# Optimization experiments

Measured on AMD Instinct MI355X. Metric: run time of the kernel, lower is better.

Reference implementation:

```python
import jax, jax.numpy as jnp
import numpy as np

CANVAS = 28      # canvas_size
P = 2            # num_paths
S = 3            # num_segments
PPP = S * 3 + 1  # points_per_path = 10
T = 32           # samples per bezier segment
SS = 2           # 2x2 = 4 supersamples per pixel (num_samples=4)
MARGIN = 2.0
TAU = 0.5        # anti-alias softness of coverage (differentiable rasterizer)
LATENT = 64
HIDDEN = 512


def _leaky(x):
    return jnp.where(x >= 0, x, 0.2 * x)


def _encoder(x, e_w1, e_b1, e_w2, e_b2, w_mu, b_mu, w_lv, b_lv):
    h = x.reshape(x.shape[0], -1)
    h = _leaky(h @ e_w1 + e_b1)
    h = _leaky(h @ e_w2 + e_b2)
    return h @ w_mu + b_mu, h @ w_lv + b_lv


def _decoder(z, d_w1, d_b1, d_w2, d_b2, p_w, p_b, wd_w, wd_b, a_w, a_b):
    B = z.shape[0]
    h = jax.nn.selu(z @ d_w1 + d_b1)
    h = jax.nn.selu(h @ d_w2 + d_b2)
    pts = jnp.tanh(h @ p_w + p_b).reshape(B, P, PPP, 2)
    pts = pts * (CANVAS / 2 - MARGIN) + CANVAS / 2
    # stack overlapping cubic segments: [B,P,S,4,2]
    cp = jnp.stack([pts[:, :, 3 * s:3 * s + 4, :] for s in range(S)], axis=2)
    widths = jax.nn.sigmoid(h @ wd_w + wd_b) * 2.0 + 1.0  # [B,P]
    alphas = jax.nn.sigmoid(h @ a_w + a_b)                # [B,P]
    return cp, widths, alphas


def _render(cp, widths, alphas):
    """Differentiable supersampled stroke rasterizer, white bg, 1-x flip."""
    B = cp.shape[0]
    t = (jnp.arange(T, dtype=cp.dtype) + 0.5) / T
    basis = jnp.stack([(1 - t) ** 3, 3 * t * (1 - t) ** 2,
                       3 * t ** 2 * (1 - t), t ** 3], axis=-1)  # [T,4]
    curve = jnp.einsum('tk,bpskc->bpstc', basis, cp).reshape(B, P, S * T, 2)
    # supersampled pixel sample positions (pixel units)
    coords = (jnp.arange(CANVAS * SS, dtype=cp.dtype) + 0.5) / SS
    ys, xs = jnp.meshgrid(coords, coords, indexing='ij')
    samp = jnp.stack([xs, ys], -1).reshape(-1, 2)  # [N,2], N = (28*2)^2
    # [B,P,N,M] squared distances -> min over curve samples
    d2 = jnp.sum((samp[None, None, :, None, :] - curve[:, :, None, :, :]) ** 2, -1)
    d = jnp.sqrt(jnp.min(d2, axis=-1) + 1e-12)  # [B,P,N]
    cov = jax.nn.sigmoid((widths[..., None] * 0.5 - d) / TAU)
    a = alphas[..., None] * cov                 # per-path ink opacity
    val = jnp.prod(1.0 - a, axis=1)             # composite black ink over bg=1.0
    img = val.reshape(B, CANVAS, SS, CANVAS, SS).mean(axis=(2, 4))
    return 1.0 - img[:, None]                   # [B,1,H,W]


def setup_inputs() -> dict:
    key = jax.random.key(0)
    ks = jax.random.split(key, 24)
    n = lambda k, s, sc=0.05: (jax.random.normal(k, s, dtype=jnp.float32) * sc)
    B = 128
    return {
        'x': jax.random.uniform(ks[0], (B, 1, 28, 28), dtype=jnp.float32),
        'eps': jax.random.normal(ks[1], (B, LATENT), dtype=jnp.float32),
        'e_w1': n(ks[2], (784, 256)), 'e_b1': jnp.zeros(256),
        'e_w2': n(ks[3], (256, 256)), 'e_b2': jnp.zeros(256),
        'w_mu': n(ks[4], (256, LATENT)), 'b_mu': jnp.zeros(LATENT),
        'w_lv': n(ks[5], (256, LATENT)), 'b_lv': jnp.zeros(LATENT),
        'd_w1': n(ks[6], (LATENT, HIDDEN)), 'd_b1': jnp.zeros(HIDDEN),
        'd_w2': n(ks[7], (HIDDEN, HIDDEN)), 'd_b2': jnp.zeros(HIDDEN),
        'p_w': n(ks[8], (HIDDEN, P * PPP * 2)), 'p_b': jnp.zeros(P * PPP * 2),
        'wd_w': n(ks[9], (HIDDEN, P)), 'wd_b': jnp.zeros(P),
        'a_w': n(ks[10], (HIDDEN, P)), 'a_b': jnp.zeros(P),
    }


def reference(x, eps, e_w1, e_b1, e_w2, e_b2, w_mu, b_mu, w_lv, b_lv,
              d_w1, d_b1, d_w2, d_b2, p_w, p_b, wd_w, wd_b, a_w, a_b):
    mu, logvar = _encoder(x, e_w1, e_b1, e_w2, e_b2, w_mu, b_mu, w_lv, b_lv)
    z = mu + eps * jnp.exp(0.5 * logvar)
    cp, widths, alphas = _decoder(z, d_w1, d_b1, d_w2, d_b2,
                                  p_w, p_b, wd_w, wd_b, a_w, a_b)
    rendered = _render(cp, widths, alphas)
    return rendered, mu, logvar, cp, widths, alphas
```

## Files before the change

kernel.cpp:

```cpp
#include <hip/hip_runtime.h>
#include <hip/hip_bf16.h>
#include <math.h>

#define REND_OFF 0
#define MU_OFF   100352
#define LV_OFF   108544
#define CP_OFF   116736
#define W_OFF    122880
#define A_OFF    123136

#define Q_W1 0
#define Q_W2 25600
#define Q_ML 33792
#define Q_D1 37888
#define Q_D2 41984
#define Q_H  74752
#define Q_TOT 78848

__device__ __forceinline__ float leakyf(float x) {
    return x >= 0.f ? x : 0.2f * x;
}
__device__ __forceinline__ float seluf(float x) {
    const float sc = 1.0507009873554805f;
    const float al = 1.6732632423543772f;
    return x > 0.f ? sc * x : sc * al * expm1f(x);
}
__device__ __forceinline__ float sigmoidf(float x) {
    return 1.f / (1.f + expf(-x));
}
__device__ __forceinline__ void bf2(unsigned u, float& lo, float& hi) {
    lo = __uint_as_float(u << 16);
    hi = __uint_as_float(u & 0xffff0000u);
}
__device__ __forceinline__ unsigned short bfbits(float v) {
    __hip_bfloat16 h = (__hip_bfloat16)v;
    return *(unsigned short*)&h;
}

__global__ __launch_bounds__(256) void conv_w(
    const float* __restrict__ e_w1, const float* __restrict__ e_w2,
    const float* __restrict__ w_mu, const float* __restrict__ w_lv,
    const float* __restrict__ d_w1, const float* __restrict__ d_w2,
    const float* __restrict__ p_w,  const float* __restrict__ wd_w,
    const float* __restrict__ a_w,  uint4* __restrict__ wsq)
{
    int t = blockIdx.x * 256 + threadIdx.x;
    if (t >= Q_TOT) return;
    float v[8];
    if (t < Q_W2) {
        int q = t, k2 = q >> 6, j4 = q & 63;
        int k0 = 2 * k2, c0 = 4 * j4;
        #pragma unroll
        for (int e = 0; e < 8; ++e) {
            int k = k0 + (e >> 2), c = c0 + (e & 3);
            v[e] = (k < 784) ? e_w1[k * 256 + c] : 0.f;
        }
    } else if (t < Q_ML) {
        int q = t - Q_W2, k2 = q >> 6, j4 = q & 63;
        int k0 = 2 * k2, c0 = 4 * j4;
        #pragma unroll
        for (int e = 0; e < 8; ++e)
            v[e] = e_w2[(k0 + (e >> 2)) * 256 + c0 + (e & 3)];
    } else if (t < Q_D1) {
        int q = t - Q_ML, k2 = q >> 5, j4 = q & 31;
        int k0 = 2 * k2, c0 = 4 * j4;
        #pragma unroll
        for (int e = 0; e < 8; ++e) {
            int k = k0 + (e >> 2), c = c0 + (e & 3);
            v[e] = (c < 64) ? w_mu[k * 64 + c] : w_lv[k * 64 + c - 64];
        }
    } else if (t < Q_D2) {
        int q = t - Q_D1, k2 = q >> 7, j4 = q & 127;
        int k0 = 2 * k2, c0 = 4 * j4;
        #pragma unroll
        for (int e = 0; e < 8; ++e)
            v[e] = d_w1[(k0 + (e >> 2)) * 512 + c0 + (e & 3)];
    } else if (t < Q_H) {
        int q = t - Q_D2, k2 = q >> 7, j4 = q & 127;
        int k0 = 2 * k2, c0 = 4 * j4;
        #pragma unroll
        for (int e = 0; e < 8; ++e)
            v[e] = d_w2[(k0 + (e >> 2)) * 512 + c0 + (e & 3)];
    } else {
        int q = t - Q_H, k2 = q >> 4, j4 = q & 15;
        int k0 = 2 * k2, c0 = 4 * j4;
        #pragma unroll
        for (int e = 0; e < 8; ++e) {
            int k = k0 + (e >> 2), c = c0 + (e & 3);
            v[e] = (c < 40) ? p_w[k * 40 + c]
                 : (c < 42) ? wd_w[k * 2 + c - 40]
                 : (c < 44) ? a_w[k * 2 + c - 42] : 0.f;
        }
    }
    uint4 u;
    u.x = bfbits(v[0]) | ((unsigned)bfbits(v[1]) << 16);
    u.y = bfbits(v[2]) | ((unsigned)bfbits(v[3]) << 16);
    u.z = bfbits(v[4]) | ((unsigned)bfbits(v[5]) << 16);
    u.w = bfbits(v[6]) | ((unsigned)bfbits(v[7]) << 16);
    wsq[t] = u;
}

template<int K2, int N, int JG, int S, int KsP>
__device__ __forceinline__ void layer_gemm(const uint4* __restrict__ wq,
                                           const float4* __restrict__ xq,
                                           float* __restrict__ red, int tid)
{
    constexpr int NTp = N + 4;
    const int jg = tid % JG, ks = tid / JG;
    const uint4* wp = wq + (ks * KsP) * (N / 4) + jg;
    const float4* xp = xq + ks * KsP;
    float a00=0,a01=0,a02=0,a03=0, a10=0,a11=0,a12=0,a13=0;
    #pragma unroll 8
    for (int kk = 0; kk < KsP; ++kk) {
        uint4 w = wp[kk * (N / 4)];
        float4 xv = xp[kk];
        float w0,w1,w2,w3,w4,w5,w6,w7;
        bf2(w.x,w0,w1); bf2(w.y,w2,w3); bf2(w.z,w4,w5); bf2(w.w,w6,w7);
        a00=fmaf(xv.x,w0,a00); a01=fmaf(xv.x,w1,a01);
        a02=fmaf(xv.x,w2,a02); a03=fmaf(xv.x,w3,a03);
        a10=fmaf(xv.y,w0,a10); a11=fmaf(xv.y,w1,a11);
        a12=fmaf(xv.y,w2,a12); a13=fmaf(xv.y,w3,a13);
        a00=fmaf(xv.z,w4,a00); a01=fmaf(xv.z,w5,a01);
        a02=fmaf(xv.z,w6,a02); a03=fmaf(xv.z,w7,a03);
        a10=fmaf(xv.w,w4,a10); a11=fmaf(xv.w,w5,a11);
        a12=fmaf(xv.w,w6,a12); a13=fmaf(xv.w,w7,a13);
    }
    *(float4*)&red[(0 * S + ks) * NTp + 4 * jg] = make_float4(a00,a01,a02,a03);
    *(float4*)&red[(1 * S + ks) * NTp + 4 * jg] = make_float4(a10,a11,a12,a13);
}

template<int N, int S, int ACT>
__device__ __forceinline__ void layer_reduce(const float* __restrict__ red,
                                             const float* __restrict__ bias,
                                             float* __restrict__ Cint, int tid)
{
    constexpr int NTp = N + 4;
    if (tid < 2 * N) {
        int b = tid / N, j = tid % N;
        float s = bias[j];
        #pragma unroll
        for (int si = 0; si < S; ++si) s += red[(b * S + si) * NTp + j];
        s = (ACT == 1) ? leakyf(s) : seluf(s);
        Cint[j * 2 + b] = s;
    }
}

__global__ __launch_bounds__(1024) void vae_mlp(
    const float* __restrict__ x,    const float* __restrict__ eps,
    const float* __restrict__ e_b1, const float* __restrict__ e_b2,
    const float* __restrict__ b_mu, const float* __restrict__ b_lv,
    const float* __restrict__ d_b1, const float* __restrict__ d_b2,
    const float* __restrict__ p_b,  const float* __restrict__ wd_b,
    const float* __restrict__ a_b,
    const uint4* __restrict__ wsq,  float* __restrict__ out)
{
    const int b0  = blockIdx.x * 2;
    const int tid = threadIdx.x;

    __shared__ __align__(16) float xs[1600];
    __shared__ __align__(16) float h1i[512];
    __shared__ __align__(16) float h2i[512];
    __shared__ __align__(16) float zsi[128];
    __shared__ __align__(16) float hd1i[1024];
    __shared__ __align__(16) float hd2i[1024];
    __shared__ float mulv[2][128];
    __shared__ float pts[2][40];
    __shared__ __align__(16) float red[8704];

    for (int i = tid; i < 1600; i += 1024) {
        int k = i >> 1, b = i & 1;
        xs[i] = (k < 784) ? x[(b0 + b) * 784 + k] : 0.f;
    }
    __syncthreads();

    layer_gemm<400, 256, 64, 16, 25>(wsq + Q_W1, (const float4*)xs, red, tid);
    __syncthreads();
    layer_reduce<256, 16, 1>(red, e_b1, h1i, tid);
    __syncthreads();

    layer_gemm<128, 256, 64, 16, 8>(wsq + Q_W2, (const float4*)h1i, red, tid);
    __syncthreads();
    layer_reduce<256, 16, 1>(red, e_b2, h2i, tid);
    __syncthreads();

    layer_gemm<128, 128, 32, 32, 4>(wsq + Q_ML, (const float4*)h2i, red, tid);
    __syncthreads();
    if (tid < 256) {
        int b = tid >> 7, u = tid & 127;
        float s = (u < 64) ? b_mu[u] : b_lv[u - 64];
        #pragma unroll
        for (int si = 0; si < 32; ++si) s += red[(b * 32 + si) * 132 + u];
        mulv[b][u] = s;
        out[(u < 64 ? MU_OFF : LV_OFF) + (b0 + b) * 64 + (u & 63)] = s;
    }
    __syncthreads();
    if (tid < 128) {
        int b = tid >> 6, j = tid & 63;
        zsi[j * 2 + b] = fmaf(eps[(b0 + b) * 64 + j],
                              expf(0.5f * mulv[b][64 + j]), mulv[b][j]);
    }
    __syncthreads();

    layer_gemm<32, 512, 128, 8, 4>(wsq + Q_D1, (const float4*)zsi, red, tid);
    __syncthreads();
    layer_reduce<512, 8, 2>(red, d_b1, hd1i, tid);
    __syncthreads();

    layer_gemm<256, 512, 128, 8, 32>(wsq + Q_D2, (const float4*)hd1i, red, tid);
    __syncthreads();
    layer_reduce<512, 8, 2>(red, d_b2, hd2i, tid);
    __syncthreads();

    layer_gemm<256, 64, 16, 64, 4>(wsq + Q_H, (const float4*)hd2i, red, tid);
    __syncthreads();
    if (tid < 128) {
        int b = tid >> 6, u = tid & 63;
        if (u < 44) {
            float s = 0.f;
            #pragma unroll
            for (int si = 0; si < 64; ++si) s += red[(b * 64 + si) * 68 + u];
            if (u < 40) {
                pts[b][u] = tanhf(s + p_b[u]) * 12.f + 14.f;
            } else if (u < 42) {
                out[W_OFF + (b0 + b) * 2 + (u - 40)] =
                    sigmoidf(s + wd_b[u - 40]) * 2.f + 1.f;
            } else {
                out[A_OFF + (b0 + b) * 2 + (u - 42)] = sigmoidf(s + a_b[u - 42]);
            }
        }
    }
    __syncthreads();

    if (tid < 96) {
        int bs = tid / 48, i = tid % 48;
        int p = i / 24, rem = i % 24;
        int s = rem / 8, kc = rem % 8;
        int k = kc >> 1, c = kc & 1;
        out[CP_OFF + (b0 + bs) * 48 + i] = pts[bs][p * 20 + (3 * s + k) * 2 + c];
    }
}

__global__ __launch_bounds__(256) void vae_render(float* __restrict__ out)
{
    const int b   = blockIdx.x;
    const int q   = blockIdx.y;
    const int tid = threadIdx.x;

    __shared__ float2 cur[192];
    __shared__ float  wa[4];

    if (tid < 192) {
        int p = tid / 96;
        int m = tid % 96;
        int s = m / 32;
        int t = m % 32;
        float u  = (t + 0.5f) * (1.f / 32.f);
        float v  = 1.f - u;
        float b0 = v * v * v;
        float b1 = 3.f * u * v * v;
        float b2 = 3.f * u * u * v;
        float b3 = u * u * u;
        const float* cp = out + CP_OFF + b * 48 + p * 24 + s * 8;
        float cx = b0 * cp[0] + b1 * cp[2] + b2 * cp[4] + b3 * cp[6];
        float cy = b0 * cp[1] + b1 * cp[3] + b2 * cp[5] + b3 * cp[7];
        cur[tid] = make_float2(cx, cy);
    } else if (tid < 196) {
        int i = tid - 192;
        wa[i] = (i < 2) ? 0.5f * out[W_OFF + b * 2 + i]
                        : out[A_OFF + b * 2 + (i - 2)];
    }
    __syncthreads();

    if (tid < 196) {
        int Y = tid / 28, X = tid - Y * 28;
        float px0 = X + 0.25f;
        float py0 = (7 * q + Y) + 0.25f;

        float mA[4] = {1e30f, 1e30f, 1e30f, 1e30f};
        float mB[4] = {1e30f, 1e30f, 1e30f, 1e30f};
        #pragma unroll 4
        for (int m = 0; m < 96; ++m) {
            float2 c = cur[m];
            float dx0 = px0 - c.x, dy0 = py0 - c.y;
            float dx1 = dx0 + 0.5f, dy1 = dy0 + 0.5f;
            float xx0 = dx0 * dx0, xx1 = dx1 * dx1;
            float yy0 = dy0 * dy0, yy1 = dy1 * dy1;
            mA[0] = fminf(mA[0], xx0 + yy0);
            mA[1] = fminf(mA[1], xx1 + yy0);
            mA[2] = fminf(mA[2], xx0 + yy1);
            mA[3] = fminf(mA[3], xx1 + yy1);
        }
        #pragma unroll 4
        for (int m = 96; m < 192; ++m) {
            float2 c = cur[m];
            float dx0 = px0 - c.x, dy0 = py0 - c.y;
            float dx1 = dx0 + 0.5f, dy1 = dy0 + 0.5f;
            float xx0 = dx0 * dx0, xx1 = dx1 * dx1;
            float yy0 = dy0 * dy0, yy1 = dy1 * dy1;
            mB[0] = fminf(mB[0], xx0 + yy0);
            mB[1] = fminf(mB[1], xx1 + yy0);
            mB[2] = fminf(mB[2], xx0 + yy1);
            mB[3] = fminf(mB[3], xx1 + yy1);
        }

        const float w0 = wa[0], w1 = wa[1], a0 = wa[2], a1 = wa[3];
        float v = 0.f;
        #pragma unroll
        for (int s = 0; s < 4; ++s) {
            float d0 = sqrtf(mA[s] + 1e-12f);
            float d1 = sqrtf(mB[s] + 1e-12f);
            float c0 = a0 / (1.f + expf(-2.f * (w0 - d0)));
            float c1 = a1 / (1.f + expf(-2.f * (w1 - d1)));
            v += (1.f - c0) * (1.f - c1);
        }
        out[REND_OFF + b * 784 + (7 * q + Y) * 28 + X] = 1.f - 0.25f * v;
    }
}

extern "C" void kernel_launch(void* const* d_in, const int* in_sizes, int n_in,
                              void* d_out, int out_size, void* d_ws, size_t ws_size,
                              hipStream_t stream) {
    const float* x    = (const float*)d_in[0];
    const float* eps  = (const float*)d_in[1];
    const float* e_w1 = (const float*)d_in[2];
    const float* e_b1 = (const float*)d_in[3];
    const float* e_w2 = (const float*)d_in[4];
    const float* e_b2 = (const float*)d_in[5];
    const float* w_mu = (const float*)d_in[6];
    const float* b_mu = (const float*)d_in[7];
    const float* w_lv = (const float*)d_in[8];
    const float* b_lv = (const float*)d_in[9];
    const float* d_w1 = (const float*)d_in[10];
    const float* d_b1 = (const float*)d_in[11];
    const float* d_w2 = (const float*)d_in[12];
    const float* d_b2 = (const float*)d_in[13];
    const float* p_w  = (const float*)d_in[14];
    const float* p_b  = (const float*)d_in[15];
    const float* wd_w = (const float*)d_in[16];
    const float* wd_b = (const float*)d_in[17];
    const float* a_w  = (const float*)d_in[18];
    const float* a_b  = (const float*)d_in[19];
    float* out = (float*)d_out;
    uint4* wsq = (uint4*)d_ws;

    hipLaunchKernelGGL(conv_w, dim3((Q_TOT + 255) / 256), dim3(256), 0, stream,
                       e_w1, e_w2, w_mu, w_lv, d_w1, d_w2, p_w, wd_w, a_w, wsq);
    hipLaunchKernelGGL(vae_mlp, dim3(64), dim3(1024), 0, stream,
                       x, eps, e_b1, e_b2, b_mu, b_lv, d_b1, d_b2,
                       p_b, wd_b, a_b, wsq, out);
    hipLaunchKernelGGL(vae_render, dim3(128, 4), dim3(256), 0, stream, out);
}
```

Baseline: 125.5 us.

## Switch MLP to fp16 packed dot2 and process one sample per block

Weights are now stored as fp16 pairs along K instead of bf16 pairs along N. Activations are packed into fp16 pairs, and the GEMM inner loop uses the v_dot2 fp32-accumulate intrinsic. Each block now handles one batch sample instead of two, which doubles the grid to 128 blocks and halves per-block work and shared memory. This is meant to cut ALU work and spread the serial MLP chain across more CUs, but weight traffic per sample doubles and fp16 range and precision differ from bf16.

```diff
diff --git a/kernel.cpp b/kernel.cpp
--- a/kernel.cpp
+++ b/kernel.cpp
@@ -1,5 +1,6 @@
 #include <hip/hip_runtime.h>
 #include <hip/hip_bf16.h>
+#include <hip/hip_fp16.h>
 #include <math.h>
 
 #define REND_OFF 0
@@ -17,6 +18,8 @@
 #define Q_H  74752
 #define Q_TOT 78848
 
+typedef _Float16 half2_t __attribute__((ext_vector_type(2)));
+
 __device__ __forceinline__ float leakyf(float x) {
     return x >= 0.f ? x : 0.2f * x;
 }
@@ -28,13 +31,21 @@
 __device__ __forceinline__ float sigmoidf(float x) {
     return 1.f / (1.f + expf(-x));
 }
-__device__ __forceinline__ void bf2(unsigned u, float& lo, float& hi) {
-    lo = __uint_as_float(u << 16);
-    hi = __uint_as_float(u & 0xffff0000u);
-}
-__device__ __forceinline__ unsigned short bfbits(float v) {
-    __hip_bfloat16 h = (__hip_bfloat16)v;
-    return *(unsigned short*)&h;
+__device__ __forceinline__ unsigned pkh(float a, float b) {
+    __half ha = __float2half(a), hb = __float2half(b);
+    return (unsigned)__half_as_ushort(ha) | ((unsigned)__half_as_ushort(hb) << 16);
+}
+__device__ __forceinline__ half2_t as_h2(unsigned u) {
+    union { unsigned u; half2_t h; } c; c.u = u; return c.h;
+}
+__device__ __forceinline__ float dot2(unsigned a, unsigned w, float acc) {
+#if __has_builtin(__builtin_amdgcn_fdot2)
+    return __builtin_amdgcn_fdot2(as_h2(a), as_h2(w), acc, false);
+#else
+    half2_t ah = as_h2(a), wh = as_h2(w);
+    acc = fmaf((float)ah[0], (float)wh[0], acc);
+    return fmaf((float)ah[1], (float)wh[1], acc);
+#endif
 }
 
 __global__ __launch_bounds__(256) void conv_w(
@@ -46,102 +57,110 @@
 {
     int t = blockIdx.x * 256 + threadIdx.x;
     if (t >= Q_TOT) return;
-    float v[8];
+    float lo[4], hi[4];
     if (t < Q_W2) {
         int q = t, k2 = q >> 6, j4 = q & 63;
         int k0 = 2 * k2, c0 = 4 * j4;
         #pragma unroll
-        for (int e = 0; e < 8; ++e) {
-            int k = k0 + (e >> 2), c = c0 + (e & 3);
-            v[e] = (k < 784) ? e_w1[k * 256 + c] : 0.f;
+        for (int c = 0; c < 4; ++c) {
+            lo[c] = (k0     < 784) ? e_w1[k0 * 256 + c0 + c] : 0.f;
+            hi[c] = (k0 + 1 < 784) ? e_w1[(k0 + 1) * 256 + c0 + c] : 0.f;
         }
     } else if (t < Q_ML) {
         int q = t - Q_W2, k2 = q >> 6, j4 = q & 63;
         int k0 = 2 * k2, c0 = 4 * j4;
         #pragma unroll
-        for (int e = 0; e < 8; ++e)
-            v[e] = e_w2[(k0 + (e >> 2)) * 256 + c0 + (e & 3)];
+        for (int c = 0; c < 4; ++c) {
+            lo[c] = e_w2[k0 * 256 + c0 + c];
+            hi[c] = e_w2[(k0 + 1) * 256 + c0 + c];
+        }
     } else if (t < Q_D1) {
         int q = t - Q_ML, k2 = q >> 5, j4 = q & 31;
         int k0 = 2 * k2, c0 = 4 * j4;
         #pragma unroll
-        for (int e = 0; e < 8; ++e) {
-            int k = k0 + (e >> 2), c = c0 + (e & 3);
-            v[e] = (c < 64) ? w_mu[k * 64 + c] : w_lv[k * 64 + c - 64];
+        for (int c = 0; c < 4; ++c) {
+            int cc = c0 + c;
+            lo[c] = (cc < 64) ? w_mu[k0 * 64 + cc] : w_lv[k0 * 64 + cc - 64];
+            hi[c] = (cc < 64) ? w_mu[(k0 + 1) * 64 + cc]
+                              : w_lv[(k0 + 1) * 64 + cc - 64];
         }
     } else if (t < Q_D2) {
         int q = t - Q_D1, k2 = q >> 7, j4 = q & 127;
         int k0 = 2 * k2, c0 = 4 * j4;
         #pragma unroll
-        for (int e = 0; e < 8; ++e)
-            v[e] = d_w1[(k0 + (e >> 2)) * 512 + c0 + (e & 3)];
+        for (int c = 0; c < 4; ++c) {
+            lo[c] = d_w1[k0 * 512 + c0 + c];
+            hi[c] = d_w1[(k0 + 1) * 512 + c0 + c];
+        }
     } else if (t < Q_H) {
         int q = t - Q_D2, k2 = q >> 7, j4 = q & 127;
         int k0 = 2 * k2, c0 = 4 * j4;
         #pragma unroll
-        for (int e = 0; e < 8; ++e)
-            v[e] = d_w2[(k0 + (e >> 2)) * 512 + c0 + (e & 3)];
+        for (int c = 0; c < 4; ++c) {
+            lo[c] = d_w2[k0 * 512 + c0 + c];
+            hi[c] = d_w2[(k0 + 1) * 512 + c0 + c];
+        }
     } else {
         int q = t - Q_H, k2 = q >> 4, j4 = q & 15;
         int k0 = 2 * k2, c0 = 4 * j4;
         #pragma unroll
-        for (int e = 0; e < 8; ++e) {
-            int k = k0 + (e >> 2), c = c0 + (e & 3);
-            v[e] = (c < 40) ? p_w[k * 40 + c]
-                 : (c < 42) ? wd_w[k * 2 + c - 40]
-                 : (c < 44) ? a_w[k * 2 + c - 42] : 0.f;
+        for (int c = 0; c < 4; ++c) {
+            int cc = c0 + c;
+            lo[c] = (cc < 40) ? p_w[k0 * 40 + cc]
+                  : (cc < 42) ? wd_w[k0 * 2 + cc - 40]
+                  : (cc < 44) ? a_w[k0 * 2 + cc - 42] : 0.f;
+            hi[c] = (cc < 40) ? p_w[(k0 + 1) * 40 + cc]
+                  : (cc < 42) ? wd_w[(k0 + 1) * 2 + cc - 40]
+                  : (cc < 44) ? a_w[(k0 + 1) * 2 + cc - 42] : 0.f;
         }
     }
     uint4 u;
-    u.x = bfbits(v[0]) | ((unsigned)bfbits(v[1]) << 16);
-    u.y = bfbits(v[2]) | ((unsigned)bfbits(v[3]) << 16);
-    u.z = bfbits(v[4]) | ((unsigned)bfbits(v[5]) << 16);
-    u.w = bfbits(v[6]) | ((unsigned)bfbits(v[7]) << 16);
+    u.x = pkh(lo[0], hi[0]);
+    u.y = pkh(lo[1], hi[1]);
+    u.z = pkh(lo[2], hi[2]);
+    u.w = pkh(lo[3], hi[3]);
     wsq[t] = u;
 }
 
-template<int K2, int N, int JG, int S, int KsP>
-__device__ __forceinline__ void layer_gemm(const uint4* __restrict__ wq,
-                                           const float4* __restrict__ xq,
-                                           float* __restrict__ red, int tid)
+template<int N, int JG, int S, int Ks>
+__device__ __forceinline__ void hgemm(const uint4* __restrict__ wq,
+                                      const unsigned* __restrict__ xu,
+                                      float* __restrict__ red, int tid)
 {
     constexpr int NTp = N + 4;
     const int jg = tid % JG, ks = tid / JG;
-    const uint4* wp = wq + (ks * KsP) * (N / 4) + jg;
-    const float4* xp = xq + ks * KsP;
-    float a00=0,a01=0,a02=0,a03=0, a10=0,a11=0,a12=0,a13=0;
+    const uint4* wp = wq + (ks * Ks) * (N / 4) + jg;
+    const unsigned* xp = xu + ks * Ks;
+    float a0 = 0.f, a1 = 0.f, a2 = 0.f, a3 = 0.f;
     #pragma unroll 8
-    for (int kk = 0; kk < KsP; ++kk) {
+    for (int kk = 0; kk < Ks; ++kk) {
         uint4 w = wp[kk * (N / 4)];
-        float4 xv = xp[kk];
-        float w0,w1,w2,w3,w4,w5,w6,w7;
-        bf2(w.x,w0,w1); bf2(w.y,w2,w3); bf2(w.z,w4,w5); bf2(w.w,w6,w7);
-        a00=fmaf(xv.x,w0,a00); a01=fmaf(xv.x,w1,a01);
-        a02=fmaf(xv.x,w2,a02); a03=fmaf(xv.x,w3,a03);
-        a10=fmaf(xv.y,w0,a10); a11=fmaf(xv.y,w1,a11);
-        a12=fmaf(xv.y,w2,a12); a13=fmaf(xv.y,w3,a13);
-        a00=fmaf(xv.z,w4,a00); a01=fmaf(xv.z,w5,a01);
-        a02=fmaf(xv.z,w6,a02); a03=fmaf(xv.z,w7,a03);
-        a10=fmaf(xv.w,w4,a10); a11=fmaf(xv.w,w5,a11);
-        a12=fmaf(xv.w,w6,a12); a13=fmaf(xv.w,w7,a13);
-    }
-    *(float4*)&red[(0 * S + ks) * NTp + 4 * jg] = make_float4(a00,a01,a02,a03);
-    *(float4*)&red[(1 * S + ks) * NTp + 4 * jg] = make_float4(a10,a11,a12,a13);
+        unsigned av = xp[kk];
+        a0 = dot2(av, w.x, a0);
+        a1 = dot2(av, w.y, a1);
+        a2 = dot2(av, w.z, a2);
+        a3 = dot2(av, w.w, a3);
+    }
+    *(float4*)&red[ks * NTp + 4 * jg] = make_float4(a0, a1, a2, a3);
 }
 
 template<int N, int S, int ACT>
-__device__ __forceinline__ void layer_reduce(const float* __restrict__ red,
-                                             const float* __restrict__ bias,
-                                             float* __restrict__ Cint, int tid)
+__device__ __forceinline__ void reduce_pack(const float* __restrict__ red,
+                                            const float* __restrict__ bias,
+                                            unsigned* __restrict__ Cu, int tid)
 {
     constexpr int NTp = N + 4;
-    if (tid < 2 * N) {
-        int b = tid / N, j = tid % N;
-        float s = bias[j];
-        #pragma unroll
-        for (int si = 0; si < S; ++si) s += red[(b * S + si) * NTp + j];
-        s = (ACT == 1) ? leakyf(s) : seluf(s);
-        Cint[j * 2 + b] = s;
+    if (tid < N / 2) {
+        int j0 = 2 * tid;
+        float s0 = bias[j0], s1 = bias[j0 + 1];
+        #pragma unroll
+        for (int si = 0; si < S; ++si) {
+            s0 += red[si * NTp + j0];
+            s1 += red[si * NTp + j0 + 1];
+        }
+        if (ACT == 1) { s0 = leakyf(s0); s1 = leakyf(s1); }
+        else          { s0 = seluf(s0);  s1 = seluf(s1);  }
+        Cu[tid] = pkh(s0, s1);
     }
 }
 
@@ -154,89 +173,94 @@
     const float* __restrict__ a_b,
     const uint4* __restrict__ wsq,  float* __restrict__ out)
 {
-    const int b0  = blockIdx.x * 2;
+    const int b   = blockIdx.x;
     const int tid = threadIdx.x;
 
-    __shared__ __align__(16) float xs[1600];
-    __shared__ __align__(16) float h1i[512];
-    __shared__ __align__(16) float h2i[512];
-    __shared__ __align__(16) float zsi[128];
-    __shared__ __align__(16) float hd1i[1024];
-    __shared__ __align__(16) float hd2i[1024];
-    __shared__ float mulv[2][128];
-    __shared__ float pts[2][40];
-    __shared__ __align__(16) float red[8704];
-
-    for (int i = tid; i < 1600; i += 1024) {
-        int k = i >> 1, b = i & 1;
-        xs[i] = (k < 784) ? x[(b0 + b) * 784 + k] : 0.f;
-    }
-    __syncthreads();
-
-    layer_gemm<400, 256, 64, 16, 25>(wsq + Q_W1, (const float4*)xs, red, tid);
-    __syncthreads();
-    layer_reduce<256, 16, 1>(red, e_b1, h1i, tid);
-    __syncthreads();
-
-    layer_gemm<128, 256, 64, 16, 8>(wsq + Q_W2, (const float4*)h1i, red, tid);
-    __syncthreads();
-    layer_reduce<256, 16, 1>(red, e_b2, h2i, tid);
-    __syncthreads();
-
-    layer_gemm<128, 128, 32, 32, 4>(wsq + Q_ML, (const float4*)h2i, red, tid);
-    __syncthreads();
-    if (tid < 256) {
-        int b = tid >> 7, u = tid & 127;
-        float s = (u < 64) ? b_mu[u] : b_lv[u - 64];
-        #pragma unroll
-        for (int si = 0; si < 32; ++si) s += red[(b * 32 + si) * 132 + u];
-        mulv[b][u] = s;
-        out[(u < 64 ? MU_OFF : LV_OFF) + (b0 + b) * 64 + (u & 63)] = s;
-    }
-    __syncthreads();
-    if (tid < 128) {
-        int b = tid >> 6, j = tid & 63;
-        zsi[j * 2 + b] = fmaf(eps[(b0 + b) * 64 + j],
-                              expf(0.5f * mulv[b][64 + j]), mulv[b][j]);
-    }
-    __syncthreads();
-
-    layer_gemm<32, 512, 128, 8, 4>(wsq + Q_D1, (const float4*)zsi, red, tid);
-    __syncthreads();
-    layer_reduce<512, 8, 2>(red, d_b1, hd1i, tid);
-    __syncthreads();
-
-    layer_gemm<256, 512, 128, 8, 32>(wsq + Q_D2, (const float4*)hd1i, red, tid);
-    __syncthreads();
-    layer_reduce<512, 8, 2>(red, d_b2, hd2i, tid);
-    __syncthreads();
-
-    layer_gemm<256, 64, 16, 64, 4>(wsq + Q_H, (const float4*)hd2i, red, tid);
-    __syncthreads();
-    if (tid < 128) {
-        int b = tid >> 6, u = tid & 63;
-        if (u < 44) {
-            float s = 0.f;
-            #pragma unroll
-            for (int si = 0; si < 64; ++si) s += red[(b * 64 + si) * 68 + u];
-            if (u < 40) {
-                pts[b][u] = tanhf(s + p_b[u]) * 12.f + 14.f;
-            } else if (u < 42) {
-                out[W_OFF + (b0 + b) * 2 + (u - 40)] =
-                    sigmoidf(s + wd_b[u - 40]) * 2.f + 1.f;
-            } else {
-                out[A_OFF + (b0 + b) * 2 + (u - 42)] = sigmoidf(s + a_b[u - 42]);
-            }
-        }
-    }
-    __syncthreads();
-
-    if (tid < 96) {
-        int bs = tid / 48, i = tid % 48;
-        int p = i / 24, rem = i % 24;
+    __shared__ __align__(16) unsigned xs[400];
+    __shared__ __align__(16) unsigned h1u[128];
+    __shared__ __align__(16) unsigned h2u[128];
+    __shared__ __align__(16) unsigned zu[32];
+    __shared__ __align__(16) unsigned d1u[256];
+    __shared__ __align__(16) unsigned d2u[256];
+    __shared__ float mulv[128];
+    __shared__ float pts[40];
+    __shared__ __align__(16) float red[4352];
+
+    if (tid < 400) {
+        int k0 = 2 * tid;
+        float x0 = (k0     < 784) ? x[b * 784 + k0] : 0.f;
+        float x1 = (k0 + 1 < 784) ? x[b * 784 + k0 + 1] : 0.f;
+        xs[tid] = pkh(x0, x1);
+    }
+    __syncthreads();
+
+    hgemm<256, 64, 16, 25>(wsq + Q_W1, xs, red, tid);
+    __syncthreads();
+    reduce_pack<256, 16, 1>(red, e_b1, h1u, tid);
+    __syncthreads();
+
+    hgemm<256, 64, 16, 8>(wsq + Q_W2, h1u, red, tid);
+    __syncthreads();
+    reduce_pack<256, 16, 1>(red, e_b2, h2u, tid);
+    __syncthreads();
+
+    hgemm<128, 32, 32, 4>(wsq + Q_ML, h2u, red, tid);
+    __syncthreads();
+    if (tid < 64) {
+        int u0 = 2 * tid;
+        float s0 = (u0 < 64) ? b_mu[u0] : b_lv[u0 - 64];
+        float s1 = (u0 < 64) ? b_mu[u0 + 1] : b_lv[u0 + 1 - 64];
+        #pragma unroll
+        for (int si = 0; si < 32; ++si) {
+            s0 += red[si * 132 + u0];
+            s1 += red[si * 132 + u0 + 1];
+        }
+        mulv[u0] = s0; mulv[u0 + 1] = s1;
+        int base = (u0 < 64) ? MU_OFF : LV_OFF;
+        out[base + b * 64 + (u0 & 63)]     = s0;
+        out[base + b * 64 + (u0 & 63) + 1] = s1;
+    }
+    __syncthreads();
+    if (tid < 32) {
+        int j0 = 2 * tid;
+        float z0 = fmaf(eps[b * 64 + j0],     expf(0.5f * mulv[64 + j0]),     mulv[j0]);
+        float z1 = fmaf(eps[b * 64 + j0 + 1], expf(0.5f * mulv[64 + j0 + 1]), mulv[j0 + 1]);
+        zu[tid] = pkh(z0, z1);
+    }
+    __syncthreads();
+
+    hgemm<512, 128, 8, 4>(wsq + Q_D1, zu, red, tid);
+    __syncthreads();
+    reduce_pack<512, 8, 2>(red, d_b1, d1u, tid);
+    __syncthreads();
+
+    hgemm<512, 128, 8, 32>(wsq + Q_D2, d1u, red, tid);
+    __syncthreads();
+    reduce_pack<512, 8, 2>(red, d_b2, d2u, tid);
+    __syncthreads();
+
+    hgemm<64, 16, 64, 4>(wsq + Q_H, d2u, red, tid);
+    __syncthreads();
+    if (tid < 44) {
+        float s = 0.f;
+        #pragma unroll
+        for (int si = 0; si < 64; ++si) s += red[si * 68 + tid];
+        if (tid < 40) {
+            pts[tid] = tanhf(s + p_b[tid]) * 12.f + 14.f;
+        } else if (tid < 42) {
+            out[W_OFF + b * 2 + (tid - 40)] =
+                sigmoidf(s + wd_b[tid - 40]) * 2.f + 1.f;
+        } else {
+            out[A_OFF + b * 2 + (tid - 42)] = sigmoidf(s + a_b[tid - 42]);
+        }
+    }
+    __syncthreads();
+
+    if (tid < 48) {
+        int p = tid / 24, rem = tid % 24;
         int s = rem / 8, kc = rem % 8;
         int k = kc >> 1, c = kc & 1;
-        out[CP_OFF + (b0 + bs) * 48 + i] = pts[bs][p * 20 + (3 * s + k) * 2 + c];
+        out[CP_OFF + b * 48 + tid] = pts[p * 20 + (3 * s + k) * 2 + c];
     }
 }
 
@@ -345,7 +369,7 @@
 
     hipLaunchKernelGGL(conv_w, dim3((Q_TOT + 255) / 256), dim3(256), 0, stream,
                        e_w1, e_w2, w_mu, w_lv, d_w1, d_w2, p_w, wd_w, a_w, wsq);
-    hipLaunchKernelGGL(vae_mlp, dim3(64), dim3(1024), 0, stream,
+    hipLaunchKernelGGL(vae_mlp, dim3(128), dim3(1024), 0, stream,
                        x, eps, e_b1, e_b2, b_mu, b_lv, d_b1, d_b2,
                        p_b, wd_b, a_b, wsq, out);
     hipLaunchKernelGGL(vae_render, dim3(128, 4), dim3(256), 0, stream, out);
```

Result: no change. 123.7 us, median of 2 (-1.4%).
